# Kernel optimization log

Hardware: AMD Instinct MI355X
Metric: run time of the kernel (lower is better)

Reference implementation:

```python
import jax, jax.numpy as jnp
import numpy as np
import math

B, TH, STEPS = 4, 120, 8
D_IN, D_MODEL, N_HEADS, N_LAYERS, D_FF = 32, 512, 8, 4, 2048
N_SUB = 5
D_HEAD = D_MODEL // N_HEADS
EPS = 1e-5


def _pos_encoding(T, d):
    pos = jnp.arange(T, dtype=jnp.float32)[:, None]
    div = jnp.exp(jnp.arange(0, d, 2, dtype=jnp.float32) * (-math.log(10000.0) / d))
    pe = jnp.zeros((T, d), dtype=jnp.float32)
    pe = pe.at[:, 0::2].set(jnp.sin(pos * div))
    pe = pe.at[:, 1::2].set(jnp.cos(pos * div))
    return pe


def setup_inputs() -> dict:
    key = jax.random.key(0)
    ks = jax.random.split(key, 16)
    s = 0.02
    n = lambda k, shp: jax.random.normal(k, shp, jnp.float32) * s
    return {
        "history": jax.random.normal(ks[0], (B, TH, D_IN), jnp.float32),
        "steps": STEPS,
        "W_emb": n(ks[1], (D_MODEL, D_IN)),
        "b_emb": jnp.zeros((D_MODEL,), jnp.float32),
        "Wq": n(ks[2], (N_LAYERS, D_MODEL, D_MODEL)),
        "Wk": n(ks[3], (N_LAYERS, D_MODEL, D_MODEL)),
        "Wv": n(ks[4], (N_LAYERS, D_MODEL, D_MODEL)),
        "Wo": n(ks[5], (N_LAYERS, D_MODEL, D_MODEL)),
        "ln1_g": jnp.ones((N_LAYERS, D_MODEL), jnp.float32),
        "ln1_b": jnp.zeros((N_LAYERS, D_MODEL), jnp.float32),
        "W1": n(ks[6], (N_LAYERS, D_FF, D_MODEL)),
        "b1": jnp.zeros((N_LAYERS, D_FF), jnp.float32),
        "W2": n(ks[7], (N_LAYERS, D_MODEL, D_FF)),
        "b2": jnp.zeros((N_LAYERS, D_MODEL), jnp.float32),
        "ln2_g": jnp.ones((N_LAYERS, D_MODEL), jnp.float32),
        "ln2_b": jnp.zeros((N_LAYERS, D_MODEL), jnp.float32),
        "Wr1": n(ks[8], (D_FF, 2 * D_MODEL)),
        "br1": jnp.zeros((D_FF,), jnp.float32),
        "Wr2": n(ks[9], (D_IN, D_FF)),
        "br2": jnp.zeros((D_IN,), jnp.float32),
    }


def _layernorm(x, g, b):
    mu = x.mean(-1, keepdims=True)
    var = ((x - mu) ** 2).mean(-1, keepdims=True)
    return (x - mu) / jnp.sqrt(var + EPS) * g + b


def reference(history, steps, W_emb, b_emb, Wq, Wk, Wv, Wo, ln1_g, ln1_b,
              W1, b1, W2, b2, ln2_g, ln2_b, Wr1, br1, Wr2, br2):
    total_len = TH + steps
    pe = _pos_encoding(total_len, D_MODEL)
    idx = jnp.arange(total_len)
    # NOTE: faithful to source: mask True where kv index > q index (equinox: True = attend)
    mask = idx[:, None] < idx[None, :]
    neg = jnp.finfo(jnp.float32).min
    scale = math.sqrt(D_MODEL)

    def transformer(buf):  # buf: [T, D_IN] -> [T, D_MODEL]
        h = (buf @ W_emb.T + b_emb) * scale + pe
        for l in range(N_LAYERS):
            q = (h @ Wq[l].T).reshape(total_len, N_HEADS, D_HEAD)
            k = (h @ Wk[l].T).reshape(total_len, N_HEADS, D_HEAD)
            v = (h @ Wv[l].T).reshape(total_len, N_HEADS, D_HEAD)
            logits = jnp.einsum("qhd,khd->hqk", q, k) / math.sqrt(D_HEAD)
            logits = jnp.where(mask[None], logits, neg)
            w = jax.nn.softmax(logits, axis=-1)
            attn = jnp.einsum("hqk,khd->qhd", w, v).reshape(total_len, D_MODEL)
            h = _layernorm(h + attn @ Wo[l].T, ln1_g[l], ln1_b[l])
            m = jax.nn.gelu(h @ W1[l].T + b1[l]) @ W2[l].T + b2[l]
            h = _layernorm(h + m, ln2_g[l], ln2_b[l])
        return h

    def refine(start_val, ctx):  # start_val: [D_IN], ctx: [D_MODEL]
        def body(i, cur):
            we = (W_emb @ cur + b_emb) * scale
            comb = jnp.concatenate([we, ctx])
            delta = Wr2 @ jax.nn.gelu(Wr1 @ comb + br1) + br2
            return cur + delta
        return jax.lax.fori_loop(0, N_SUB, body, start_val)

    def single(hist):  # [TH, D_IN] -> [steps, D_IN]
        buf = jnp.zeros((total_len, D_IN), jnp.float32).at[:TH].set(hist)

        def scan_fn(buf, step_idx):
            h = transformer(buf)  # full recompute each decode step (no KV cache)
            ptr = TH + step_idx
            next_val = refine(buf[ptr - 1], h[ptr - 1])
            return buf.at[ptr].set(next_val), next_val

        _, preds = jax.lax.scan(scan_fn, buf, jnp.arange(steps))
        return preds

    return jax.vmap(single)(history)
```

## Files before the change

### kernel.cpp

```cpp
#include <hip/hip_runtime.h>
#include <math.h>

namespace {
constexpr int NB = 4;
constexpr int SEQ = 128;
constexpr int TH_ = 120;
constexpr int NSTEP = 8;
constexpr int DMODEL = 512;
constexpr int NHEAD = 8;
constexpr int DHEAD = 64;
constexpr int DFFN = 2048;
constexpr int DIN = 32;
constexpr int MROWS = NB*SEQ;
constexpr float SCALE_EMB = 22.627416997969522f;
constexpr float LN_EPS = 1e-5f;
constexpr float NEGF = -3.4028234663852886e38f;
constexpr float PE_C = -0.017988946039015984f;
}

using short8 = __attribute__((ext_vector_type(8))) short;
using f32x4  = __attribute__((ext_vector_type(4))) float;

__device__ __forceinline__ float wave_sum(float v){
#pragma unroll
  for(int off=32;off;off>>=1) v += __shfl_xor(v,off,64);
  return v;
}
__device__ __forceinline__ float blk_sum(float v, float* scr){
  v = wave_sum(v);
  __syncthreads();
  if((threadIdx.x&63)==0) scr[threadIdx.x>>6]=v;
  __syncthreads();
  return scr[0]+scr[1]+scr[2]+scr[3];
}
__device__ __forceinline__ float gelu_t(float x){
  float t = 0.7978845608028654f*(x + 0.044715f*x*x*x);
  return 0.5f*x*(1.0f + tanhf(t));
}
__device__ __forceinline__ float pe_val(int t, int d){
  float div = expf((float)(d & ~1) * PE_C);
  float a = (float)t * div;
  return (d & 1) ? cosf(a) : sinf(a);
}
__device__ __forceinline__ unsigned short f2b(float f){
  union { float f; unsigned u; } c; c.f = f;
  unsigned u = c.u + 0x7FFFu + ((c.u>>16)&1u);
  return (unsigned short)(u>>16);
}
__device__ __forceinline__ short8 pack8(const float* f){
  short8 s;
#pragma unroll
  for(int i=0;i<8;i++) s[i] = (short)f2b(f[i]);
  return s;
}

__global__ __launch_bounds__(256) void conv_w(const float* __restrict__ Wq,
                                              const float* __restrict__ Wk,
                                              const float* __restrict__ Wv,
                                              const float* __restrict__ Wo,
                                              const float* __restrict__ W1,
                                              const float* __restrict__ W2,
                                              unsigned short* __restrict__ dst){
  size_t base = ((size_t)blockIdx.x*256 + threadIdx.x)*8;
  if(base >= 12582912u) return;
  const float* src; size_t off;
  if(base < 1048576u){ src=Wq; off=base; }
  else if(base < 2097152u){ src=Wk; off=base-1048576u; }
  else if(base < 3145728u){ src=Wv; off=base-2097152u; }
  else if(base < 4194304u){ src=Wo; off=base-3145728u; }
  else if(base < 8388608u){ src=W1; off=base-4194304u; }
  else { src=W2; off=base-8388608u; }
  float4 a = *(const float4*)(src+off);
  float4 b = *(const float4*)(src+off+4);
  float f[8] = {a.x,a.y,a.z,a.w,b.x,b.y,b.z,b.w};
  *(short8*)(dst + base) = pack8(f);
}

__global__ __launch_bounds__(256) void init_h0(const float* __restrict__ hist,
                                               const float* __restrict__ W_emb,
                                               const float* __restrict__ b_emb,
                                               float* __restrict__ h0,
                                               unsigned short* __restrict__ h0b){
  int bt = blockIdx.x;
  int b = bt >> 7, t = bt & 127;
  __shared__ float x[DIN];
  if(threadIdx.x < DIN)
    x[threadIdx.x] = (t < TH_) ? hist[((size_t)b*TH_ + t)*DIN + threadIdx.x] : 0.f;
  __syncthreads();
  for(int d = threadIdx.x; d < DMODEL; d += 256){
    float s = 0.f;
#pragma unroll 8
    for(int i=0;i<DIN;i++) s += W_emb[d*DIN+i]*x[i];
    float v = SCALE_EMB*(s + b_emb[d]) + pe_val(t,d);
    h0[(size_t)bt*DMODEL + d] = v;
    h0b[(size_t)bt*DMODEL + d] = f2b(v);
  }
}

__global__ __launch_bounds__(256) void init_misc(const float* __restrict__ Wr1,
                                                 const float* __restrict__ W_emb,
                                                 const float* __restrict__ b_emb,
                                                 const float* __restrict__ br1,
                                                 const float* __restrict__ hist,
                                                 float* __restrict__ M1,
                                                 float* __restrict__ cb1,
                                                 float* __restrict__ cur_x){
  __shared__ float row[DMODEL];
  int j0 = blockIdx.x*8;
  for(int jj=0;jj<8;jj++){
    int j = j0+jj;
    for(int k=threadIdx.x;k<DMODEL;k+=256) row[k] = Wr1[(size_t)j*1024 + k];
    __syncthreads();
    if(threadIdx.x < DIN){
      int i = threadIdx.x; float s = 0.f;
      for(int k=0;k<DMODEL;k++) s += row[k]*W_emb[k*DIN+i];
      M1[j*DIN+i] = SCALE_EMB*s;
    } else if(threadIdx.x == DIN){
      float s=0.f;
      for(int k=0;k<DMODEL;k++) s += row[k]*b_emb[k];
      cb1[j] = br1[j] + SCALE_EMB*s;
    }
    __syncthreads();
  }
  if(blockIdx.x==0 && threadIdx.x<NB*DIN){
    int b = threadIdx.x>>5, i = threadIdx.x&31;
    cur_x[b*DIN+i] = hist[((size_t)b*TH_ + (TH_-1))*DIN + i];
  }
}

template<int LNM>
__global__ __launch_bounds__(256,1) void gemm_k(
    const unsigned short* __restrict__ A16, int Ka,
    const unsigned short* __restrict__ Wa,
    const unsigned short* __restrict__ Wb,
    const unsigned short* __restrict__ Wc,
    const float* __restrict__ bias, const float* __restrict__ resid,
    const float* __restrict__ lnx, const float* __restrict__ lng,
    const float* __restrict__ lnbta,
    float* __restrict__ Cf, unsigned short* __restrict__ Cb,
    int c_rs, int c_mode, int act)
{
  __shared__ __align__(16) unsigned short As[64][72];
  __shared__ __align__(16) unsigned short Bs[128][72];
  __shared__ float Smu[64], Srs[64];
  __shared__ float Sgs[DMODEL], Scs[DMODEL];

  int bx = blockIdx.x, by = blockIdx.y;
  int n0 = bx*128;
  int m0 = by*64;
  int tid = threadIdx.x, w = tid>>6, ln = tid&63;

  const unsigned short* Wsrc; int nrow0;
  if(c_mode==2){ int which = n0>>9; Wsrc = (which==0?Wa:(which==1?Wb:Wc)); nrow0 = n0&511; }
  else { Wsrc = Wa; nrow0 = n0; }

  if constexpr(LNM != 0){
    float4 xr[16][2];
#pragma unroll
    for(int rr=0;rr<16;rr++){
      const float* xp = lnx + (size_t)(m0 + w*16 + rr)*DMODEL + ln*8;
      xr[rr][0] = *(const float4*)xp;
      xr[rr][1] = *(const float4*)(xp+4);
    }
    if constexpr(LNM==1){
      for(int k=tid;k<DMODEL;k+=256){ Sgs[k]=lng[k]; Scs[k]=lnbta[k]; }
    }
#pragma unroll
    for(int rr=0;rr<16;rr++){
      float f[8] = {xr[rr][0].x,xr[rr][0].y,xr[rr][0].z,xr[rr][0].w,
                    xr[rr][1].x,xr[rr][1].y,xr[rr][1].z,xr[rr][1].w};
      float s = 0.f;
#pragma unroll
      for(int i=0;i<8;i++) s += f[i];
      s = wave_sum(s);
      float mu = s*(1.f/DMODEL);
      float v2 = 0.f;
#pragma unroll
      for(int i=0;i<8;i++){ float d0=f[i]-mu; v2 += d0*d0; }
      v2 = wave_sum(v2);
      float rsv = rsqrtf(v2*(1.f/DMODEL) + LN_EPS);
      if(ln==0){ Smu[w*16+rr]=mu; Srs[w*16+rr]=rsv; }
    }
    __syncthreads();
  }

  f32x4 acc[4][2];
#pragma unroll
  for(int i=0;i<4;i++)
#pragma unroll
    for(int j=0;j<2;j++) acc[i][j] = (f32x4){0.f,0.f,0.f,0.f};

  int fr = ln&15, fq = (ln>>4)*8;
  int arow = tid>>2, akq = (tid&3)*16;
  int brow = tid>>1, bkq = (tid&1)*32;

  float amu=0.f, ars=0.f;
  if constexpr(LNM==1){ amu = Smu[arow]; ars = Srs[arow]; }

  short8 a0, a1;
  float4 t0, t1, t2, t3;
  short8 b0, b1, b2, b3;

  auto LOADB = [&](int k0){
    const unsigned short* bp = Wsrc + (size_t)(nrow0+brow)*Ka + k0 + bkq;
    b0 = *(const short8*)bp;
    b1 = *(const short8*)(bp+8);
    b2 = *(const short8*)(bp+16);
    b3 = *(const short8*)(bp+24);
  };
  auto LOADA = [&](int k0){
    if constexpr(LNM==1){
      const float* fp = lnx + (size_t)(m0+arow)*DMODEL + k0 + akq;
      t0 = *(const float4*)fp;
      t1 = *(const float4*)(fp+4);
      t2 = *(const float4*)(fp+8);
      t3 = *(const float4*)(fp+12);
    } else {
      const unsigned short* ap = A16 + (size_t)(m0+arow)*Ka + k0 + akq;
      a0 = *(const short8*)ap;
      a1 = *(const short8*)(ap+8);
    }
  };

  LOADA(0); LOADB(0);
  for(int k0=0;k0<Ka;k0+=64){
    if constexpr(LNM==1){
      float tt[16] = {t0.x,t0.y,t0.z,t0.w, t1.x,t1.y,t1.z,t1.w,
                      t2.x,t2.y,t2.z,t2.w, t3.x,t3.y,t3.z,t3.w};
      float o[16];
#pragma unroll
      for(int i=0;i<16;i++){
        int c = k0 + akq + i;
        o[i] = (tt[i]-amu)*ars*Sgs[c] + Scs[c];
      }
      *(short8*)&As[arow][akq]   = pack8(o);
      *(short8*)&As[arow][akq+8] = pack8(o+8);
    } else {
      *(short8*)&As[arow][akq]   = a0;
      *(short8*)&As[arow][akq+8] = a1;
    }
    *(short8*)&Bs[brow][bkq]    = b0;
    *(short8*)&Bs[brow][bkq+8]  = b1;
    *(short8*)&Bs[brow][bkq+16] = b2;
    *(short8*)&Bs[brow][bkq+24] = b3;
    __syncthreads();
    if(k0+64 < Ka){ LOADA(k0+64); LOADB(k0+64); }
    short8 af[4][2], bf[2][2];
#pragma unroll
    for(int kf=0;kf<2;kf++){
#pragma unroll
      for(int rt=0;rt<4;rt++) af[rt][kf] = *(const short8*)&As[rt*16 + fr][kf*32 + fq];
#pragma unroll
      for(int ct=0;ct<2;ct++) bf[ct][kf] = *(const short8*)&Bs[32*w + ct*16 + fr][kf*32 + fq];
    }
#pragma unroll
    for(int kf=0;kf<2;kf++)
#pragma unroll
      for(int rt=0;rt<4;rt++)
#pragma unroll
        for(int ct=0;ct<2;ct++)
          acc[rt][ct] = __builtin_amdgcn_mfma_f32_16x16x32_bf16(af[rt][kf], bf[ct][kf], acc[rt][ct], 0, 0, 0);
    __syncthreads();
  }

  float rv[4][2][4];
  const float* rsrc = (LNM==2) ? lnx : resid;
  if(rsrc){
#pragma unroll
    for(int rt=0;rt<4;rt++)
#pragma unroll
      for(int ct=0;ct<2;ct++){
        int n = n0 + 32*w + ct*16 + fr;
        int row0 = m0 + rt*16 + (ln>>4)*4;
        const float* p = rsrc + (size_t)row0*DMODEL + n;
#pragma unroll
        for(int r=0;r<4;r++) rv[rt][ct][r] = p[(size_t)r*DMODEL];
      }
  }

#pragma unroll
  for(int rt=0;rt<4;rt++){
#pragma unroll
    for(int ct=0;ct<2;ct++){
      int n = n0 + 32*w + ct*16 + fr;
      int ri0 = rt*16 + (ln>>4)*4;
      int row0 = m0 + ri0;
#pragma unroll
      for(int r=0;r<4;r++){
        int ri = ri0 + r;
        int row = row0 + r;
        float v = acc[rt][ct][r];
        if(bias)  v += bias[n];
        if constexpr(LNM==2){
          v += (rv[rt][ct][r] - Smu[ri])*Srs[ri]*lng[n] + lnbta[n];
        } else {
          if(rsrc) v += rv[rt][ct][r];
        }
        if(act==1) v = gelu_t(v);
        if(c_mode==0)      Cf[(size_t)row*c_rs + n] = v;
        else if(c_mode==1) Cb[(size_t)row*c_rs + n] = f2b(v);
        else {
          int which = n>>9, rem = n&511;
          int b = row>>7, t = row&127;
          Cf[(size_t)which*(MROWS*DMODEL) +
             ((size_t)(b*NHEAD + (rem>>6))*SEQ + t)*DHEAD + (rem&63)] = v;
        }
      }
    }
  }
}

__global__ __launch_bounds__(256) void attn_k(const float* __restrict__ qb,
                                              const float* __restrict__ kb,
                                              const float* __restrict__ vb,
                                              unsigned short* __restrict__ attb){
  int b = blockIdx.z, h = blockIdx.y;
  int r0 = blockIdx.x*32;
  const float* Kh = kb + (size_t)(b*NHEAD+h)*SEQ*DHEAD;
  const float* Vh = vb + (size_t)(b*NHEAD+h)*SEQ*DHEAD;
  const float* Qh = qb + (size_t)(b*NHEAD+h)*SEQ*DHEAD;
  __shared__ float kv[SEQ][DHEAD];
  __shared__ float wsm[32][132];
  __shared__ float qs[32][68];
  int tid = threadIdx.x;
  int kk = tid>>4, d4 = (tid&15)*4;

  {
    float4 t[8];
#pragma unroll
    for(int i=0;i<8;i++) t[i] = *(const float4*)(Kh + (size_t)(kk+16*i)*DHEAD + d4);
    float4 q0 = *(const float4*)(Qh + (size_t)(r0+kk)*DHEAD + d4);
    float4 q1 = *(const float4*)(Qh + (size_t)(r0+kk+16)*DHEAD + d4);
#pragma unroll
    for(int i=0;i<8;i++){ int k = kk+16*i; *(float4*)&kv[k][d4 ^ (k&60)] = t[i]; }
    *(float4*)&qs[kk   ][d4] = q0;
    *(float4*)&qs[kk+16][d4] = q1;
  }
  __syncthreads();

  {
    int rp = tid>>4;
    int kg = tid&15;
    float acc[2][8];
#pragma unroll
    for(int i=0;i<2;i++)
#pragma unroll
      for(int kk2=0;kk2<8;kk2++) acc[i][kk2]=0.f;
#pragma unroll 4
    for(int dd=0;dd<16;dd++){
      float4 q0 = *(const float4*)&qs[2*rp][dd*4];
      float4 q1 = *(const float4*)&qs[2*rp+1][dd*4];
#pragma unroll
      for(int kk2=0;kk2<8;kk2++){
        int k = 8*kg + kk2;
        int off = (dd*4) ^ (k&60);
        float4 kv4 = *(const float4*)&kv[k][off];
        acc[0][kk2] += q0.x*kv4.x + q0.y*kv4.y + q0.z*kv4.z + q0.w*kv4.w;
        acc[1][kk2] += q1.x*kv4.x + q1.y*kv4.y + q1.z*kv4.z + q1.w*kv4.w;
      }
    }
#pragma unroll
    for(int i=0;i<2;i++){
      int t = r0 + 2*rp + i;
#pragma unroll
      for(int kk2=0;kk2<8;kk2++){
        int k = 8*kg + kk2;
        wsm[2*rp+i][k] = (k > t) ? acc[i][kk2]*0.125f : NEGF;
      }
    }
  }
  __syncthreads();

  {
    int l2 = tid&63, wv = tid>>6;
    for(int r=wv;r<32;r+=4){
      float l0 = wsm[r][l2], l1 = wsm[r][l2+64];
      float m = fmaxf(l0,l1);
#pragma unroll
      for(int off=32;off;off>>=1) m = fmaxf(m, __shfl_xor(m,off,64));
      float e0 = expf(l0-m), e1 = expf(l1-m);
      float s = e0+e1;
      s = wave_sum(s);
      float inv = 1.f/s;
      wsm[r][l2] = e0*inv; wsm[r][l2+64] = e1*inv;
    }
  }
  __syncthreads();

  {
    float4 t[8];
#pragma unroll
    for(int i=0;i<8;i++) t[i] = *(const float4*)(Vh + (size_t)(kk+16*i)*DHEAD + d4);
#pragma unroll
    for(int i=0;i<8;i++) *(float4*)&kv[kk+16*i][d4] = t[i];
  }
  __syncthreads();

  {
    int dq = (tid&15)*4, rg = tid>>4;
    for(int r=rg;r<32;r+=16){
      float4 acc2 = make_float4(0.f,0.f,0.f,0.f);
      for(int k=0;k<SEQ;k++){
        float w0 = wsm[r][k];
        float4 v = *(const float4*)&kv[k][dq];
        acc2.x += w0*v.x; acc2.y += w0*v.y; acc2.z += w0*v.z; acc2.w += w0*v.w;
      }
      int row = b*SEQ + r0 + r;
      unsigned short* op = attb + (size_t)row*DMODEL + h*DHEAD + dq;
      op[0]=f2b(acc2.x); op[1]=f2b(acc2.y); op[2]=f2b(acc2.z); op[3]=f2b(acc2.w);
    }
  }
}

__global__ __launch_bounds__(256) void ctx_k(const float* __restrict__ r2,
                                             const float* __restrict__ g2,
                                             const float* __restrict__ b2,
                                             const float* __restrict__ Wr1,
                                             const float* __restrict__ cb1,
                                             float* __restrict__ ctxt, int ptr){
  int b = blockIdx.y; int j0 = blockIdx.x*128;
  __shared__ float raw[DMODEL], ctx[DMODEL], scr[4];
  int tid = threadIdx.x;
  const float* rp = r2 + (size_t)(b*SEQ + ptr-1)*DMODEL;
  for(int k=tid;k<DMODEL;k+=256) raw[k]=rp[k];
  __syncthreads();
  float s = 0.f;
  for(int k=tid;k<DMODEL;k+=256) s += raw[k];
  s = blk_sum(s, scr);
  float mu = s/(float)DMODEL;
  float v = 0.f;
  for(int k=tid;k<DMODEL;k+=256){ float d0 = raw[k]-mu; v += d0*d0; }
  v = blk_sum(v, scr);
  float rs = rsqrtf(v/(float)DMODEL + LN_EPS);
  for(int k=tid;k<DMODEL;k+=256) ctx[k] = (raw[k]-mu)*rs*g2[k] + b2[k];
  __syncthreads();
  int wv = tid>>6, l2 = tid&63;
  for(int jj=wv;jj<128;jj+=4){
    int j = j0+jj;
    const float* wp = Wr1 + (size_t)j*1024 + 512;
    float acc = 0.f;
#pragma unroll
    for(int q=0;q<8;q++){ int k = l2 + 64*q; acc += wp[k]*ctx[k]; }
    acc = wave_sum(acc);
    if(l2==0) ctxt[b*DFFN + j] = acc + cb1[j];
  }
}

__global__ __launch_bounds__(256) void refine_fin(const float* __restrict__ M1,
                                                  const float* __restrict__ ctxt,
                                                  const float* __restrict__ Wr2,
                                                  const float* __restrict__ br2,
                                                  float* __restrict__ cur_x,
                                                  const float* __restrict__ W_emb,
                                                  const float* __restrict__ b_emb,
                                                  float* __restrict__ out,
                                                  float* __restrict__ h0,
                                                  unsigned short* __restrict__ h0b,
                                                  int s, int ptr){
  int b = blockIdx.x, tid = threadIdx.x;
  __shared__ float cur[DIN], gs[DFFN], dscr[DIN];
  if(tid < DIN) cur[tid] = cur_x[b*DIN + tid];
  __syncthreads();
  for(int sub=0; sub<5; sub++){
    for(int jj=tid; jj<DFFN; jj+=256){
      float u = ctxt[b*DFFN + jj];
      const float* mp = M1 + (size_t)jj*DIN;
#pragma unroll
      for(int p=0;p<8;p++){
        float4 mv = *(const float4*)(mp + 4*p);
        u += mv.x*cur[4*p] + mv.y*cur[4*p+1] + mv.z*cur[4*p+2] + mv.w*cur[4*p+3];
      }
      gs[jj] = gelu_t(u);
    }
    __syncthreads();
    int w = tid>>6, l = tid&63;
#pragma unroll
    for(int q=0;q<8;q++){
      int i = w*8 + q;
      const float* wr = Wr2 + (size_t)i*DFFN;
      float a = 0.f;
#pragma unroll
      for(int p=0;p<8;p++){
        int j0 = p*256 + l*4;
        float4 wv = *(const float4*)(wr + j0);
        float4 gv = *(const float4*)&gs[j0];
        a += wv.x*gv.x + wv.y*gv.y + wv.z*gv.z + wv.w*gv.w;
      }
      a = wave_sum(a);
      if(l==0) dscr[i] = a;
    }
    __syncthreads();
    if(tid < DIN) cur[tid] += dscr[tid] + br2[tid];
    __syncthreads();
  }
  if(tid < DIN){
    out[(b*NSTEP + s)*DIN + tid] = cur[tid];
    cur_x[b*DIN + tid] = cur[tid];
  }
  __syncthreads();
  for(int d=tid; d<DMODEL; d+=256){
    float s2 = 0.f;
#pragma unroll 8
    for(int i=0;i<DIN;i++) s2 += W_emb[d*DIN+i]*cur[i];
    float v = SCALE_EMB*(s2 + b_emb[d]) + pe_val(ptr, d);
    size_t idx = (size_t)(b*SEQ + ptr)*DMODEL + d;
    h0[idx] = v;
    h0b[idx] = f2b(v);
  }
}

extern "C" void kernel_launch(void* const* d_in, const int* in_sizes, int n_in,
                              void* d_out, int out_size, void* d_ws, size_t ws_size,
                              hipStream_t stream) {
  (void)in_sizes; (void)n_in; (void)out_size; (void)ws_size;
  const float* hist = (const float*)d_in[0];
  const float* W_emb= (const float*)d_in[2];
  const float* b_emb= (const float*)d_in[3];
  const float* Wq   = (const float*)d_in[4];
  const float* Wk   = (const float*)d_in[5];
  const float* Wv   = (const float*)d_in[6];
  const float* Wo   = (const float*)d_in[7];
  const float* ln1g = (const float*)d_in[8];
  const float* ln1b = (const float*)d_in[9];
  const float* W1   = (const float*)d_in[10];
  const float* b1   = (const float*)d_in[11];
  const float* W2   = (const float*)d_in[12];
  const float* b2v  = (const float*)d_in[13];
  const float* ln2g = (const float*)d_in[14];
  const float* ln2b = (const float*)d_in[15];
  const float* Wr1  = (const float*)d_in[16];
  const float* br1  = (const float*)d_in[17];
  const float* Wr2  = (const float*)d_in[18];
  const float* br2  = (const float*)d_in[19];
  float* out = (float*)d_out;
  float* ws  = (float*)d_ws;

  const size_t BTD = (size_t)MROWS*DMODEL;
  const size_t BTDH = BTD/2;
  float* h0   = ws;
  unsigned short* h0b = (unsigned short*)(h0 + BTD);
  float* r2   = h0 + BTD + BTDH;
  float* hln  = r2 + BTD;
  float* hp   = hln + BTD;
  float* qb   = hp + BTD + BTDH;
  float* kb   = qb + BTD;
  float* vb   = kb + BTD;
  unsigned short* attb = (unsigned short*)(vb + BTD);
  unsigned short* fbuf16 = (unsigned short*)qb;
  float* r1   = hp;
  unsigned short* W16 = (unsigned short*)(qb + 4*BTD);
  float* after_w = qb + 4*BTD + 6291456;
  float* M1   = after_w;
  float* cb1  = M1 + (size_t)DFFN*DIN;
  float* ctxt = cb1 + DFFN;
  float* cur_x= ctxt + NB*DFFN;

  unsigned short* Wq16 = W16;
  unsigned short* Wk16 = W16 + 1048576;
  unsigned short* Wv16 = W16 + 2097152;
  unsigned short* Wo16 = W16 + 3145728;
  unsigned short* W116 = W16 + 4194304;
  unsigned short* W216 = W16 + 8388608;

  conv_w<<<dim3(6144),dim3(256),0,stream>>>(Wq,Wk,Wv,Wo,W1,W2,W16);
  init_h0<<<dim3(MROWS),dim3(256),0,stream>>>(hist,W_emb,b_emb,h0,h0b);
  init_misc<<<dim3(256),dim3(256),0,stream>>>(Wr1,W_emb,b_emb,br1,hist,M1,cb1,cur_x);

  for(int s=0;s<NSTEP;s++){
    int ptr = TH_ + s;
    for(int l=0;l<4;l++){
      const float* g2p = ln2g + (l-1)*DMODEL;
      const float* b2p = ln2b + (l-1)*DMODEL;
      const float* g1p = ln1g + l*DMODEL;
      const float* b1p = ln1b + l*DMODEL;

      if(l==0)
        gemm_k<0><<<dim3(12,8),dim3(256),0,stream>>>(h0b, DMODEL,
            Wq16 + (size_t)l*262144, Wk16 + (size_t)l*262144, Wv16 + (size_t)l*262144,
            nullptr, nullptr, nullptr, nullptr, nullptr,
            qb, nullptr, 0, 2, 0);
      else
        gemm_k<1><<<dim3(12,8),dim3(256),0,stream>>>(nullptr, DMODEL,
            Wq16 + (size_t)l*262144, Wk16 + (size_t)l*262144, Wv16 + (size_t)l*262144,
            nullptr, nullptr, r2, g2p, b2p,
            qb, nullptr, 0, 2, 0);

      attn_k<<<dim3(4,NHEAD,NB),dim3(256),0,stream>>>(qb,kb,vb,attb);

      if(l==0)
        gemm_k<0><<<dim3(4,8),dim3(256),0,stream>>>(attb, DMODEL,
            Wo16 + (size_t)l*262144, nullptr, nullptr,
            nullptr, h0, nullptr, nullptr, nullptr,
            r1, nullptr, DMODEL, 0, 0);
      else
        gemm_k<2><<<dim3(4,8),dim3(256),0,stream>>>(attb, DMODEL,
            Wo16 + (size_t)l*262144, nullptr, nullptr,
            nullptr, nullptr, r2, g2p, b2p,
            r1, nullptr, DMODEL, 0, 0);

      gemm_k<1><<<dim3(16,8),dim3(256),0,stream>>>(nullptr, DMODEL,
          W116 + (size_t)l*1048576, nullptr, nullptr,
          b1 + l*DFFN, nullptr, r1, g1p, b1p,
          nullptr, fbuf16, DFFN, 1, 1);

      gemm_k<2><<<dim3(4,8),dim3(256),0,stream>>>(fbuf16, DFFN,
          W216 + (size_t)l*1048576, nullptr, nullptr,
          b2v + l*DMODEL, nullptr, r1, g1p, b1p,
          r2, nullptr, DMODEL, 0, 0);
    }

    ctx_k<<<dim3(16,NB),dim3(256),0,stream>>>(r2, ln2g + 3*DMODEL, ln2b + 3*DMODEL,
                                              Wr1, cb1, ctxt, ptr);
    refine_fin<<<dim3(NB),dim3(256),0,stream>>>(M1, ctxt, Wr2, br2, cur_x,
                                                W_emb, b_emb, out, h0, h0b, s, ptr);
  }
}
```

Measured before the change: 4.996 ms.

## Load GEMM fragments directly from global into registers, dropping LDS staging

The GEMM kernel no longer stages A and B tiles through shared memory with barriers. Each lane now loads its MFMA fragments straight from global memory into double-buffered registers and computes without __syncthreads in the main loop. The aim is to remove LDS round trips and block-wide synchronisation, at the cost of redundant global loads, since every wave reloads the full A tile, and higher register pressure. The init_misc kernel is also reworked to compute 8 output rows in parallel instead of looping serially. The main loop processes two k-steps per iteration and assumes the iteration count is even.

```diff
diff --git a/kernel.cpp b/kernel.cpp
--- a/kernel.cpp
+++ b/kernel.cpp
@@ -105,26 +105,27 @@
                                                  float* __restrict__ M1,
                                                  float* __restrict__ cb1,
                                                  float* __restrict__ cur_x){
-  __shared__ float row[DMODEL];
+  __shared__ float rows8[8][DMODEL];
+  int tid = threadIdx.x;
   int j0 = blockIdx.x*8;
-  for(int jj=0;jj<8;jj++){
-    int j = j0+jj;
-    for(int k=threadIdx.x;k<DMODEL;k+=256) row[k] = Wr1[(size_t)j*1024 + k];
-    __syncthreads();
-    if(threadIdx.x < DIN){
-      int i = threadIdx.x; float s = 0.f;
-      for(int k=0;k<DMODEL;k++) s += row[k]*W_emb[k*DIN+i];
-      M1[j*DIN+i] = SCALE_EMB*s;
-    } else if(threadIdx.x == DIN){
-      float s=0.f;
-      for(int k=0;k<DMODEL;k++) s += row[k]*b_emb[k];
-      cb1[j] = br1[j] + SCALE_EMB*s;
-    }
-    __syncthreads();
-  }
-  if(blockIdx.x==0 && threadIdx.x<NB*DIN){
-    int b = threadIdx.x>>5, i = threadIdx.x&31;
-    cur_x[b*DIN+i] = hist[((size_t)b*TH_ + (TH_-1))*DIN + i];
+  for(int idx=tid; idx<8*DMODEL; idx+=256)
+    rows8[idx>>9][idx&511] = Wr1[(size_t)(j0+(idx>>9))*1024 + (idx&511)];
+  __syncthreads();
+  int jj = tid>>5, i = tid&31;
+  int j = j0+jj;
+  float s = 0.f;
+#pragma unroll 8
+  for(int k=0;k<DMODEL;k++) s += rows8[jj][k]*W_emb[k*DIN+i];
+  M1[j*DIN+i] = SCALE_EMB*s;
+  if(i==0){
+    float sb = 0.f;
+#pragma unroll 8
+    for(int k=0;k<DMODEL;k++) sb += rows8[jj][k]*b_emb[k];
+    cb1[j] = br1[j] + SCALE_EMB*sb;
+  }
+  if(blockIdx.x==0 && tid<NB*DIN){
+    int b = tid>>5, ii = tid&31;
+    cur_x[b*DIN+ii] = hist[((size_t)b*TH_ + (TH_-1))*DIN + ii];
   }
 }
 
@@ -140,8 +141,6 @@
     float* __restrict__ Cf, unsigned short* __restrict__ Cb,
     int c_rs, int c_mode, int act)
 {
-  __shared__ __align__(16) unsigned short As[64][72];
-  __shared__ __align__(16) unsigned short Bs[128][72];
   __shared__ float Smu[64], Srs[64];
   __shared__ float Sgs[DMODEL], Scs[DMODEL];
 
@@ -149,6 +148,7 @@
   int n0 = bx*128;
   int m0 = by*64;
   int tid = threadIdx.x, w = tid>>6, ln = tid&63;
+  int fr = ln&15, fq = (ln>>4)*8;
 
   const unsigned short* Wsrc; int nrow0;
   if(c_mode==2){ int which = n0>>9; Wsrc = (which==0?Wa:(which==1?Wb:Wc)); nrow0 = n0&511; }
@@ -184,75 +184,78 @@
     __syncthreads();
   }
 
+  float amu[4], ars[4];
+  if constexpr(LNM==1){
+#pragma unroll
+    for(int rt=0;rt<4;rt++){ amu[rt]=Smu[rt*16+fr]; ars[rt]=Srs[rt*16+fr]; }
+  }
+
   f32x4 acc[4][2];
 #pragma unroll
   for(int i=0;i<4;i++)
 #pragma unroll
     for(int j=0;j<2;j++) acc[i][j] = (f32x4){0.f,0.f,0.f,0.f};
 
-  int fr = ln&15, fq = (ln>>4)*8;
-  int arow = tid>>2, akq = (tid&3)*16;
-  int brow = tid>>1, bkq = (tid&1)*32;
-
-  float amu=0.f, ars=0.f;
-  if constexpr(LNM==1){ amu = Smu[arow]; ars = Srs[arow]; }
-
-  short8 a0, a1;
-  float4 t0, t1, t2, t3;
-  short8 b0, b1, b2, b3;
-
-  auto LOADB = [&](int k0){
-    const unsigned short* bp = Wsrc + (size_t)(nrow0+brow)*Ka + k0 + bkq;
-    b0 = *(const short8*)bp;
-    b1 = *(const short8*)(bp+8);
-    b2 = *(const short8*)(bp+16);
-    b3 = *(const short8*)(bp+24);
+  const unsigned short* aB = A16 ? (A16 + (size_t)(m0+fr)*Ka + fq) : (const unsigned short*)0;
+  const float* aF = (LNM==1) ? (lnx + (size_t)(m0+fr)*DMODEL + fq) : (const float*)0;
+  const unsigned short* bB = Wsrc + (size_t)(nrow0 + 32*w + fr)*Ka + fq;
+  const int niter = Ka >> 6;
+
+  short8 A0[4][2], A1[4][2];
+  float4 F0[4][2][2], F1[4][2][2];
+  short8 B0[2][2], B1[2][2];
+
+  auto LB0 = [&](int k0){
+#pragma unroll
+    for(int ct=0;ct<2;ct++)
+#pragma unroll
+      for(int kf=0;kf<2;kf++)
+        B0[ct][kf] = *(const short8*)(bB + (size_t)ct*16*Ka + k0 + kf*32);
   };
-  auto LOADA = [&](int k0){
+  auto LB1 = [&](int k0){
+#pragma unroll
+    for(int ct=0;ct<2;ct++)
+#pragma unroll
+      for(int kf=0;kf<2;kf++)
+        B1[ct][kf] = *(const short8*)(bB + (size_t)ct*16*Ka + k0 + kf*32);
+  };
+  auto LA0 = [&](int k0){
     if constexpr(LNM==1){
-      const float* fp = lnx + (size_t)(m0+arow)*DMODEL + k0 + akq;
-      t0 = *(const float4*)fp;
-      t1 = *(const float4*)(fp+4);
-      t2 = *(const float4*)(fp+8);
-      t3 = *(const float4*)(fp+12);
+#pragma unroll
+      for(int rt=0;rt<4;rt++)
+#pragma unroll
+        for(int kf=0;kf<2;kf++){
+          const float* p = aF + (size_t)rt*16*DMODEL + k0 + kf*32;
+          F0[rt][kf][0] = *(const float4*)p;
+          F0[rt][kf][1] = *(const float4*)(p+4);
+        }
     } else {
-      const unsigned short* ap = A16 + (size_t)(m0+arow)*Ka + k0 + akq;
-      a0 = *(const short8*)ap;
-      a1 = *(const short8*)(ap+8);
+#pragma unroll
+      for(int rt=0;rt<4;rt++)
+#pragma unroll
+        for(int kf=0;kf<2;kf++)
+          A0[rt][kf] = *(const short8*)(aB + (size_t)rt*16*Ka + k0 + kf*32);
     }
   };
-
-  LOADA(0); LOADB(0);
-  for(int k0=0;k0<Ka;k0+=64){
+  auto LA1 = [&](int k0){
     if constexpr(LNM==1){
-      float tt[16] = {t0.x,t0.y,t0.z,t0.w, t1.x,t1.y,t1.z,t1.w,
-                      t2.x,t2.y,t2.z,t2.w, t3.x,t3.y,t3.z,t3.w};
-      float o[16];
-#pragma unroll
-      for(int i=0;i<16;i++){
-        int c = k0 + akq + i;
-        o[i] = (tt[i]-amu)*ars*Sgs[c] + Scs[c];
-      }
-      *(short8*)&As[arow][akq]   = pack8(o);
-      *(short8*)&As[arow][akq+8] = pack8(o+8);
+#pragma unroll
+      for(int rt=0;rt<4;rt++)
+#pragma unroll
+        for(int kf=0;kf<2;kf++){
+          const float* p = aF + (size_t)rt*16*DMODEL + k0 + kf*32;
+          F1[rt][kf][0] = *(const float4*)p;
+          F1[rt][kf][1] = *(const float4*)(p+4);
+        }
     } else {
-      *(short8*)&As[arow][akq]   = a0;
-      *(short8*)&As[arow][akq+8] = a1;
-    }
-    *(short8*)&Bs[brow][bkq]    = b0;
-    *(short8*)&Bs[brow][bkq+8]  = b1;
-    *(short8*)&Bs[brow][bkq+16] = b2;
-    *(short8*)&Bs[brow][bkq+24] = b3;
-    __syncthreads();
-    if(k0+64 < Ka){ LOADA(k0+64); LOADB(k0+64); }
-    short8 af[4][2], bf[2][2];
-#pragma unroll
-    for(int kf=0;kf<2;kf++){
-#pragma unroll
-      for(int rt=0;rt<4;rt++) af[rt][kf] = *(const short8*)&As[rt*16 + fr][kf*32 + fq];
-#pragma unroll
-      for(int ct=0;ct<2;ct++) bf[ct][kf] = *(const short8*)&Bs[32*w + ct*16 + fr][kf*32 + fq];
-    }
+#pragma unroll
+      for(int rt=0;rt<4;rt++)
+#pragma unroll
+        for(int kf=0;kf<2;kf++)
+          A1[rt][kf] = *(const short8*)(aB + (size_t)rt*16*Ka + k0 + kf*32);
+    }
+  };
+  auto CMP = [&](short8 (&af)[4][2], short8 (&bf)[2][2]){
 #pragma unroll
     for(int kf=0;kf<2;kf++)
 #pragma unroll
@@ -260,7 +263,39 @@
 #pragma unroll
         for(int ct=0;ct<2;ct++)
           acc[rt][ct] = __builtin_amdgcn_mfma_f32_16x16x32_bf16(af[rt][kf], bf[ct][kf], acc[rt][ct], 0, 0, 0);
-    __syncthreads();
+  };
+  auto CMPF = [&](float4 (&fa)[4][2][2], short8 (&bf)[2][2], int k0){
+    short8 af[4][2];
+#pragma unroll
+    for(int kf=0;kf<2;kf++){
+      int c0 = k0 + kf*32 + fq;
+#pragma unroll
+      for(int rt=0;rt<4;rt++){
+        float o[8];
+        float4 lo = fa[rt][kf][0], hi = fa[rt][kf][1];
+        float x[8] = {lo.x,lo.y,lo.z,lo.w, hi.x,hi.y,hi.z,hi.w};
+#pragma unroll
+        for(int i=0;i<8;i++) o[i] = (x[i]-amu[rt])*ars[rt]*Sgs[c0+i] + Scs[c0+i];
+        af[rt][kf] = pack8(o);
+      }
+    }
+#pragma unroll
+    for(int kf=0;kf<2;kf++)
+#pragma unroll
+      for(int rt=0;rt<4;rt++)
+#pragma unroll
+        for(int ct=0;ct<2;ct++)
+          acc[rt][ct] = __builtin_amdgcn_mfma_f32_16x16x32_bf16(af[rt][kf], bf[ct][kf], acc[rt][ct], 0, 0, 0);
+  };
+
+  LA0(0); LB0(0);
+#pragma unroll 2
+  for(int i=0;i<niter;i+=2){
+    int k1 = (i+1)<<6;
+    LA1(k1); LB1(k1);
+    if constexpr(LNM==1) CMPF(F0, B0, i<<6); else CMP(A0, B0);
+    if(i+2<niter){ int k2=(i+2)<<6; LA0(k2); LB0(k2); }
+    if constexpr(LNM==1) CMPF(F1, B1, k1); else CMP(A1, B1);
   }
 
   float rv[4][2][4];
```

Result: slower. 6.192 ms (+23.9%).

## Fuse LayerNorm into full-row GEMM epilogues instead of consumer-side prologues

Applied to the files above, without the earlier changes.

Replaces the deferred-LayerNorm scheme, where each consumer GEMM recomputed row stats and normalized its fp32 A input, with a new gemm_row kernel. gemm_row computes all 512 output columns per 32-row block, so it can do bias, residual and LayerNorm in the epilogue and write both fp32 and bf16 outputs. Downstream GEMMs then read bf16 inputs directly, ctx_k no longer recomputes the final LayerNorm, and init_misc processes 8 Wr1 rows in parallel. The risk is that gemm_row launches only 16 blocks, which limits parallelism on a large GPU, and each block streams the whole weight matrix.

```diff
diff --git a/kernel.cpp b/kernel.cpp
--- a/kernel.cpp
+++ b/kernel.cpp
@@ -105,85 +105,50 @@
                                                  float* __restrict__ M1,
                                                  float* __restrict__ cb1,
                                                  float* __restrict__ cur_x){
-  __shared__ float row[DMODEL];
+  __shared__ float rows8[8][DMODEL];
+  int tid = threadIdx.x;
   int j0 = blockIdx.x*8;
-  for(int jj=0;jj<8;jj++){
-    int j = j0+jj;
-    for(int k=threadIdx.x;k<DMODEL;k+=256) row[k] = Wr1[(size_t)j*1024 + k];
-    __syncthreads();
-    if(threadIdx.x < DIN){
-      int i = threadIdx.x; float s = 0.f;
-      for(int k=0;k<DMODEL;k++) s += row[k]*W_emb[k*DIN+i];
-      M1[j*DIN+i] = SCALE_EMB*s;
-    } else if(threadIdx.x == DIN){
-      float s=0.f;
-      for(int k=0;k<DMODEL;k++) s += row[k]*b_emb[k];
-      cb1[j] = br1[j] + SCALE_EMB*s;
-    }
-    __syncthreads();
-  }
-  if(blockIdx.x==0 && threadIdx.x<NB*DIN){
-    int b = threadIdx.x>>5, i = threadIdx.x&31;
-    cur_x[b*DIN+i] = hist[((size_t)b*TH_ + (TH_-1))*DIN + i];
-  }
-}
-
-template<int LNM>
-__global__ __launch_bounds__(256,1) void gemm_k(
+  for(int idx=tid; idx<8*DMODEL; idx+=256)
+    rows8[idx>>9][idx&511] = Wr1[(size_t)(j0+(idx>>9))*1024 + (idx&511)];
+  __syncthreads();
+  int jj = tid>>5, i = tid&31;
+  int j = j0+jj;
+  float s = 0.f;
+#pragma unroll 8
+  for(int k=0;k<DMODEL;k++) s += rows8[jj][k]*W_emb[k*DIN+i];
+  M1[j*DIN+i] = SCALE_EMB*s;
+  if(i==0){
+    float sb = 0.f;
+#pragma unroll 8
+    for(int k=0;k<DMODEL;k++) sb += rows8[jj][k]*b_emb[k];
+    cb1[j] = br1[j] + SCALE_EMB*sb;
+  }
+  if(blockIdx.x==0 && tid<NB*DIN){
+    int b = tid>>5, ii = tid&31;
+    cur_x[b*DIN+ii] = hist[((size_t)b*TH_ + (TH_-1))*DIN + ii];
+  }
+}
+
+__global__ __launch_bounds__(256) void gemm_k(
     const unsigned short* __restrict__ A16, int Ka,
     const unsigned short* __restrict__ Wa,
     const unsigned short* __restrict__ Wb,
     const unsigned short* __restrict__ Wc,
     const float* __restrict__ bias, const float* __restrict__ resid,
-    const float* __restrict__ lnx, const float* __restrict__ lng,
-    const float* __restrict__ lnbta,
     float* __restrict__ Cf, unsigned short* __restrict__ Cb,
     int c_rs, int c_mode, int act)
 {
   __shared__ __align__(16) unsigned short As[64][72];
   __shared__ __align__(16) unsigned short Bs[128][72];
-  __shared__ float Smu[64], Srs[64];
-  __shared__ float Sgs[DMODEL], Scs[DMODEL];
-
-  int bx = blockIdx.x, by = blockIdx.y;
-  int n0 = bx*128;
-  int m0 = by*64;
+
+  int n0 = blockIdx.x*128;
+  int m0 = blockIdx.y*64;
   int tid = threadIdx.x, w = tid>>6, ln = tid&63;
 
   const unsigned short* Wsrc; int nrow0;
   if(c_mode==2){ int which = n0>>9; Wsrc = (which==0?Wa:(which==1?Wb:Wc)); nrow0 = n0&511; }
   else { Wsrc = Wa; nrow0 = n0; }
 
-  if constexpr(LNM != 0){
-    float4 xr[16][2];
-#pragma unroll
-    for(int rr=0;rr<16;rr++){
-      const float* xp = lnx + (size_t)(m0 + w*16 + rr)*DMODEL + ln*8;
-      xr[rr][0] = *(const float4*)xp;
-      xr[rr][1] = *(const float4*)(xp+4);
-    }
-    if constexpr(LNM==1){
-      for(int k=tid;k<DMODEL;k+=256){ Sgs[k]=lng[k]; Scs[k]=lnbta[k]; }
-    }
-#pragma unroll
-    for(int rr=0;rr<16;rr++){
-      float f[8] = {xr[rr][0].x,xr[rr][0].y,xr[rr][0].z,xr[rr][0].w,
-                    xr[rr][1].x,xr[rr][1].y,xr[rr][1].z,xr[rr][1].w};
-      float s = 0.f;
-#pragma unroll
-      for(int i=0;i<8;i++) s += f[i];
-      s = wave_sum(s);
-      float mu = s*(1.f/DMODEL);
-      float v2 = 0.f;
-#pragma unroll
-      for(int i=0;i<8;i++){ float d0=f[i]-mu; v2 += d0*d0; }
-      v2 = wave_sum(v2);
-      float rsv = rsqrtf(v2*(1.f/DMODEL) + LN_EPS);
-      if(ln==0){ Smu[w*16+rr]=mu; Srs[w*16+rr]=rsv; }
-    }
-    __syncthreads();
-  }
-
   f32x4 acc[4][2];
 #pragma unroll
   for(int i=0;i<4;i++)
@@ -194,57 +159,28 @@
   int arow = tid>>2, akq = (tid&3)*16;
   int brow = tid>>1, bkq = (tid&1)*32;
 
-  float amu=0.f, ars=0.f;
-  if constexpr(LNM==1){ amu = Smu[arow]; ars = Srs[arow]; }
-
-  short8 a0, a1;
-  float4 t0, t1, t2, t3;
-  short8 b0, b1, b2, b3;
-
-  auto LOADB = [&](int k0){
+  short8 a0, a1, b0, b1, b2, b3;
+  auto LOAD = [&](int k0){
+    const unsigned short* ap = A16 + (size_t)(m0+arow)*Ka + k0 + akq;
+    a0 = *(const short8*)ap;
+    a1 = *(const short8*)(ap+8);
     const unsigned short* bp = Wsrc + (size_t)(nrow0+brow)*Ka + k0 + bkq;
     b0 = *(const short8*)bp;
     b1 = *(const short8*)(bp+8);
     b2 = *(const short8*)(bp+16);
     b3 = *(const short8*)(bp+24);
   };
-  auto LOADA = [&](int k0){
-    if constexpr(LNM==1){
-      const float* fp = lnx + (size_t)(m0+arow)*DMODEL + k0 + akq;
-      t0 = *(const float4*)fp;
-      t1 = *(const float4*)(fp+4);
-      t2 = *(const float4*)(fp+8);
-      t3 = *(const float4*)(fp+12);
-    } else {
-      const unsigned short* ap = A16 + (size_t)(m0+arow)*Ka + k0 + akq;
-      a0 = *(const short8*)ap;
-      a1 = *(const short8*)(ap+8);
-    }
-  };
-
-  LOADA(0); LOADB(0);
+
+  LOAD(0);
   for(int k0=0;k0<Ka;k0+=64){
-    if constexpr(LNM==1){
-      float tt[16] = {t0.x,t0.y,t0.z,t0.w, t1.x,t1.y,t1.z,t1.w,
-                      t2.x,t2.y,t2.z,t2.w, t3.x,t3.y,t3.z,t3.w};
-      float o[16];
-#pragma unroll
-      for(int i=0;i<16;i++){
-        int c = k0 + akq + i;
-        o[i] = (tt[i]-amu)*ars*Sgs[c] + Scs[c];
-      }
-      *(short8*)&As[arow][akq]   = pack8(o);
-      *(short8*)&As[arow][akq+8] = pack8(o+8);
-    } else {
-      *(short8*)&As[arow][akq]   = a0;
-      *(short8*)&As[arow][akq+8] = a1;
-    }
+    *(short8*)&As[arow][akq]   = a0;
+    *(short8*)&As[arow][akq+8] = a1;
     *(short8*)&Bs[brow][bkq]    = b0;
     *(short8*)&Bs[brow][bkq+8]  = b1;
     *(short8*)&Bs[brow][bkq+16] = b2;
     *(short8*)&Bs[brow][bkq+24] = b3;
     __syncthreads();
-    if(k0+64 < Ka){ LOADA(k0+64); LOADB(k0+64); }
+    if(k0+64 < Ka) LOAD(k0+64);
     short8 af[4][2], bf[2][2];
 #pragma unroll
     for(int kf=0;kf<2;kf++){
@@ -263,39 +199,17 @@
     __syncthreads();
   }
 
-  float rv[4][2][4];
-  const float* rsrc = (LNM==2) ? lnx : resid;
-  if(rsrc){
-#pragma unroll
-    for(int rt=0;rt<4;rt++)
-#pragma unroll
-      for(int ct=0;ct<2;ct++){
-        int n = n0 + 32*w + ct*16 + fr;
-        int row0 = m0 + rt*16 + (ln>>4)*4;
-        const float* p = rsrc + (size_t)row0*DMODEL + n;
-#pragma unroll
-        for(int r=0;r<4;r++) rv[rt][ct][r] = p[(size_t)r*DMODEL];
-      }
-  }
-
 #pragma unroll
   for(int rt=0;rt<4;rt++){
 #pragma unroll
     for(int ct=0;ct<2;ct++){
       int n = n0 + 32*w + ct*16 + fr;
-      int ri0 = rt*16 + (ln>>4)*4;
-      int row0 = m0 + ri0;
 #pragma unroll
       for(int r=0;r<4;r++){
-        int ri = ri0 + r;
-        int row = row0 + r;
+        int row = m0 + rt*16 + (ln>>4)*4 + r;
         float v = acc[rt][ct][r];
         if(bias)  v += bias[n];
-        if constexpr(LNM==2){
-          v += (rv[rt][ct][r] - Smu[ri])*Srs[ri]*lng[n] + lnbta[n];
-        } else {
-          if(rsrc) v += rv[rt][ct][r];
-        }
+        if(resid) v += resid[(size_t)row*DMODEL + n];
         if(act==1) v = gelu_t(v);
         if(c_mode==0)      Cf[(size_t)row*c_rs + n] = v;
         else if(c_mode==1) Cb[(size_t)row*c_rs + n] = f2b(v);
@@ -305,6 +219,165 @@
           Cf[(size_t)which*(MROWS*DMODEL) +
              ((size_t)(b*NHEAD + (rem>>6))*SEQ + t)*DHEAD + (rem&63)] = v;
         }
+      }
+    }
+  }
+}
+
+__global__ __launch_bounds__(256,1) void gemm_row(
+    const unsigned short* __restrict__ A16, int Ka,
+    const unsigned short* __restrict__ W,
+    const float* __restrict__ bias,
+    const float* __restrict__ resid,
+    const float* __restrict__ g, const float* __restrict__ bta,
+    float* __restrict__ Yf, unsigned short* __restrict__ Yb)
+{
+  __shared__ __align__(16) unsigned short As[32][76];
+  __shared__ __align__(16) unsigned short Bs[512][76];
+  __shared__ float Ssum[32][4];
+  __shared__ float Smu[32], Srs[32];
+
+  int m0 = blockIdx.x*32;
+  int tid = threadIdx.x, w = tid>>6, ln = tid&63;
+  int fr = ln&15, fq = (ln>>4)*8;
+
+  f32x4 acc[2][8];
+#pragma unroll
+  for(int i=0;i<2;i++)
+#pragma unroll
+    for(int j=0;j<8;j++) acc[i][j] = (f32x4){0.f,0.f,0.f,0.f};
+
+  int arow = tid>>3, aoff = (tid&7)*8;
+  int brow = tid*2;
+
+  short8 aR;
+  short8 bR[16];
+  auto LOAD = [&](int k0){
+    aR = *(const short8*)(A16 + (size_t)(m0+arow)*Ka + k0 + aoff);
+    const unsigned short* p0 = W + (size_t)brow*Ka + k0;
+    const unsigned short* p1 = W + (size_t)(brow+1)*Ka + k0;
+#pragma unroll
+    for(int i=0;i<8;i++){
+      bR[i]   = *(const short8*)(p0 + i*8);
+      bR[8+i] = *(const short8*)(p1 + i*8);
+    }
+  };
+
+  LOAD(0);
+  for(int k0=0;k0<Ka;k0+=64){
+    *(short8*)&As[arow][aoff] = aR;
+#pragma unroll
+    for(int i=0;i<8;i++){
+      *(short8*)&Bs[brow  ][i*8] = bR[i];
+      *(short8*)&Bs[brow+1][i*8] = bR[8+i];
+    }
+    __syncthreads();
+    if(k0+64 < Ka) LOAD(k0+64);
+#pragma unroll
+    for(int kf=0;kf<2;kf++){
+      short8 af[2], bf[8];
+#pragma unroll
+      for(int rt=0;rt<2;rt++) af[rt] = *(const short8*)&As[rt*16 + fr][kf*32 + fq];
+#pragma unroll
+      for(int ct=0;ct<8;ct++) bf[ct] = *(const short8*)&Bs[w*128 + ct*16 + fr][kf*32 + fq];
+#pragma unroll
+      for(int rt=0;rt<2;rt++)
+#pragma unroll
+        for(int ct=0;ct<8;ct++)
+          acc[rt][ct] = __builtin_amdgcn_mfma_f32_16x16x32_bf16(af[rt], bf[ct], acc[rt][ct], 0, 0, 0);
+    }
+    __syncthreads();
+  }
+
+  float vv[2][8][4];
+#pragma unroll
+  for(int rt=0;rt<2;rt++){
+    int ri0 = rt*16 + (ln>>4)*4;
+#pragma unroll
+    for(int ct=0;ct<8;ct++){
+      int n = w*128 + ct*16 + fr;
+      float bv = bias ? bias[n] : 0.f;
+      const float* rp = resid + (size_t)(m0+ri0)*DMODEL + n;
+#pragma unroll
+      for(int r=0;r<4;r++)
+        vv[rt][ct][r] = acc[rt][ct][r] + bv + rp[(size_t)r*DMODEL];
+    }
+  }
+
+  float ps[2][4];
+#pragma unroll
+  for(int rt=0;rt<2;rt++)
+#pragma unroll
+    for(int r=0;r<4;r++){
+      float s = 0.f;
+#pragma unroll
+      for(int ct=0;ct<8;ct++) s += vv[rt][ct][r];
+      ps[rt][r] = s;
+    }
+#pragma unroll
+  for(int off=1;off<16;off<<=1)
+#pragma unroll
+    for(int rt=0;rt<2;rt++)
+#pragma unroll
+      for(int r=0;r<4;r++) ps[rt][r] += __shfl_xor(ps[rt][r], off, 64);
+  if(fr==0){
+#pragma unroll
+    for(int rt=0;rt<2;rt++)
+#pragma unroll
+      for(int r=0;r<4;r++) Ssum[rt*16 + (ln>>4)*4 + r][w] = ps[rt][r];
+  }
+  __syncthreads();
+  if(tid<32) Smu[tid] = (Ssum[tid][0]+Ssum[tid][1]+Ssum[tid][2]+Ssum[tid][3])*(1.f/DMODEL);
+  __syncthreads();
+
+  float mu_[2][4];
+#pragma unroll
+  for(int rt=0;rt<2;rt++)
+#pragma unroll
+    for(int r=0;r<4;r++) mu_[rt][r] = Smu[rt*16 + (ln>>4)*4 + r];
+
+#pragma unroll
+  for(int rt=0;rt<2;rt++)
+#pragma unroll
+    for(int r=0;r<4;r++){
+      float q = 0.f;
+#pragma unroll
+      for(int ct=0;ct<8;ct++){ float d0 = vv[rt][ct][r]-mu_[rt][r]; q += d0*d0; }
+      ps[rt][r] = q;
+    }
+#pragma unroll
+  for(int off=1;off<16;off<<=1)
+#pragma unroll
+    for(int rt=0;rt<2;rt++)
+#pragma unroll
+      for(int r=0;r<4;r++) ps[rt][r] += __shfl_xor(ps[rt][r], off, 64);
+  if(fr==0){
+#pragma unroll
+    for(int rt=0;rt<2;rt++)
+#pragma unroll
+      for(int r=0;r<4;r++) Ssum[rt*16 + (ln>>4)*4 + r][w] = ps[rt][r];
+  }
+  __syncthreads();
+  if(tid<32){
+    float v2 = (Ssum[tid][0]+Ssum[tid][1]+Ssum[tid][2]+Ssum[tid][3])*(1.f/DMODEL);
+    Srs[tid] = rsqrtf(v2 + LN_EPS);
+  }
+  __syncthreads();
+
+#pragma unroll
+  for(int rt=0;rt<2;rt++){
+    int ri0 = rt*16 + (ln>>4)*4;
+#pragma unroll
+    for(int r=0;r<4;r++){
+      int ri = ri0 + r;
+      int row = m0 + ri;
+      float rs = Srs[ri], mu = mu_[rt][r];
+#pragma unroll
+      for(int ct=0;ct<8;ct++){
+        int n = w*128 + ct*16 + fr;
+        float y = (vv[rt][ct][r]-mu)*rs*g[n] + bta[n];
+        Yf[(size_t)row*DMODEL + n] = y;
+        Yb[(size_t)row*DMODEL + n] = f2b(y);
       }
     }
   }
@@ -412,27 +485,15 @@
   }
 }
 
-__global__ __launch_bounds__(256) void ctx_k(const float* __restrict__ r2,
-                                             const float* __restrict__ g2,
-                                             const float* __restrict__ b2,
+__global__ __launch_bounds__(256) void ctx_k(const float* __restrict__ hout,
                                              const float* __restrict__ Wr1,
                                              const float* __restrict__ cb1,
                                              float* __restrict__ ctxt, int ptr){
   int b = blockIdx.y; int j0 = blockIdx.x*128;
-  __shared__ float raw[DMODEL], ctx[DMODEL], scr[4];
+  __shared__ float ctx[DMODEL];
   int tid = threadIdx.x;
-  const float* rp = r2 + (size_t)(b*SEQ + ptr-1)*DMODEL;
-  for(int k=tid;k<DMODEL;k+=256) raw[k]=rp[k];
-  __syncthreads();
-  float s = 0.f;
-  for(int k=tid;k<DMODEL;k+=256) s += raw[k];
-  s = blk_sum(s, scr);
-  float mu = s/(float)DMODEL;
-  float v = 0.f;
-  for(int k=tid;k<DMODEL;k+=256){ float d0 = raw[k]-mu; v += d0*d0; }
-  v = blk_sum(v, scr);
-  float rs = rsqrtf(v/(float)DMODEL + LN_EPS);
-  for(int k=tid;k<DMODEL;k+=256) ctx[k] = (raw[k]-mu)*rs*g2[k] + b2[k];
+  const float* rp = hout + (size_t)(b*SEQ + ptr-1)*DMODEL;
+  for(int k=tid;k<DMODEL;k+=256) ctx[k]=rp[k];
   __syncthreads();
   int wv = tid>>6, l2 = tid&63;
   for(int jj=wv;jj<128;jj+=4){
@@ -539,15 +600,16 @@
   const size_t BTDH = BTD/2;
   float* h0   = ws;
   unsigned short* h0b = (unsigned short*)(h0 + BTD);
-  float* r2   = h0 + BTD + BTDH;
-  float* hln  = r2 + BTD;
-  float* hp   = hln + BTD;
+  float* hout = h0 + BTD + BTDH;
+  float* hlnS = hout + BTD;
+  unsigned short* houtb = (unsigned short*)hlnS;
+  float* hp   = hlnS + BTD;
+  unsigned short* hpb = (unsigned short*)(hp + BTD);
   float* qb   = hp + BTD + BTDH;
   float* kb   = qb + BTD;
   float* vb   = kb + BTD;
   unsigned short* attb = (unsigned short*)(vb + BTD);
   unsigned short* fbuf16 = (unsigned short*)qb;
-  float* r1   = hp;
   unsigned short* W16 = (unsigned short*)(qb + 4*BTD);
   float* after_w = qb + 4*BTD + 6291456;
   float* M1   = after_w;
@@ -569,48 +631,29 @@
   for(int s=0;s<NSTEP;s++){
     int ptr = TH_ + s;
     for(int l=0;l<4;l++){
-      const float* g2p = ln2g + (l-1)*DMODEL;
-      const float* b2p = ln2b + (l-1)*DMODEL;
-      const float* g1p = ln1g + l*DMODEL;
-      const float* b1p = ln1b + l*DMODEL;
-
-      if(l==0)
-        gemm_k<0><<<dim3(12,8),dim3(256),0,stream>>>(h0b, DMODEL,
-            Wq16 + (size_t)l*262144, Wk16 + (size_t)l*262144, Wv16 + (size_t)l*262144,
-            nullptr, nullptr, nullptr, nullptr, nullptr,
-            qb, nullptr, 0, 2, 0);
-      else
-        gemm_k<1><<<dim3(12,8),dim3(256),0,stream>>>(nullptr, DMODEL,
-            Wq16 + (size_t)l*262144, Wk16 + (size_t)l*262144, Wv16 + (size_t)l*262144,
-            nullptr, nullptr, r2, g2p, b2p,
-            qb, nullptr, 0, 2, 0);
+      const unsigned short* Aq = (l==0)? h0b : houtb;
+      const float* resW = (l==0)? h0 : hout;
+
+      gemm_k<<<dim3(12,8),dim3(256),0,stream>>>(Aq, DMODEL,
+          Wq16 + (size_t)l*262144, Wk16 + (size_t)l*262144, Wv16 + (size_t)l*262144,
+          nullptr, nullptr, qb, nullptr, 0, 2, 0);
 
       attn_k<<<dim3(4,NHEAD,NB),dim3(256),0,stream>>>(qb,kb,vb,attb);
 
-      if(l==0)
-        gemm_k<0><<<dim3(4,8),dim3(256),0,stream>>>(attb, DMODEL,
-            Wo16 + (size_t)l*262144, nullptr, nullptr,
-            nullptr, h0, nullptr, nullptr, nullptr,
-            r1, nullptr, DMODEL, 0, 0);
-      else
-        gemm_k<2><<<dim3(4,8),dim3(256),0,stream>>>(attb, DMODEL,
-            Wo16 + (size_t)l*262144, nullptr, nullptr,
-            nullptr, nullptr, r2, g2p, b2p,
-            r1, nullptr, DMODEL, 0, 0);
-
-      gemm_k<1><<<dim3(16,8),dim3(256),0,stream>>>(nullptr, DMODEL,
+      gemm_row<<<dim3(16),dim3(256),0,stream>>>(attb, DMODEL,
+          Wo16 + (size_t)l*262144, nullptr, resW,
+          ln1g + l*DMODEL, ln1b + l*DMODEL, hp, hpb);
+
+      gemm_k<<<dim3(16,8),dim3(256),0,stream>>>(hpb, DMODEL,
           W116 + (size_t)l*1048576, nullptr, nullptr,
-          b1 + l*DFFN, nullptr, r1, g1p, b1p,
-          nullptr, fbuf16, DFFN, 1, 1);
-
-      gemm_k<2><<<dim3(4,8),dim3(256),0,stream>>>(fbuf16, DFFN,
-          W216 + (size_t)l*1048576, nullptr, nullptr,
-          b2v + l*DMODEL, nullptr, r1, g1p, b1p,
-          r2, nullptr, DMODEL, 0, 0);
-    }
-
-    ctx_k<<<dim3(16,NB),dim3(256),0,stream>>>(r2, ln2g + 3*DMODEL, ln2b + 3*DMODEL,
-                                              Wr1, cb1, ctxt, ptr);
+          b1 + l*DFFN, nullptr, nullptr, fbuf16, DFFN, 1, 1);
+
+      gemm_row<<<dim3(16),dim3(256),0,stream>>>(fbuf16, DFFN,
+          W216 + (size_t)l*1048576, b2v + l*DMODEL, hp,
+          ln2g + l*DMODEL, ln2b + l*DMODEL, hout, houtb);
+    }
+
+    ctx_k<<<dim3(16,NB),dim3(256),0,stream>>>(hout, Wr1, cb1, ctxt, ptr);
     refine_fin<<<dim3(NB),dim3(256),0,stream>>>(M1, ctxt, Wr2, br2, cur_x,
                                                 W_emb, b_emb, out, h0, h0b, s, ptr);
   }
```

After: 6.044 ms. 1.21x slower.
